# Optimization experiments

Hardware: AMD Instinct MI355X
Metric: run time of the kernel (lower is better)

## Reference

```python
import jax, jax.numpy as jnp
from jax import lax
import numpy as np

# pywt db4 filter bank (ascending order)
DEC_LO = np.array([-0.010597401784997278, 0.032883011666982945, 0.030841381835986965,
                   -0.18703481171888114, -0.02798376941698385, 0.6308807679295904,
                   0.7148465705525415, 0.23037781330885523], dtype=np.float32)
F_LEN = DEC_LO.shape[0]
_signs = ((-1.0) ** (np.arange(F_LEN) + 1)).astype(np.float32)
DEC_HI = _signs * DEC_LO[::-1]
REC_LO = DEC_LO[::-1].copy()
REC_HI = DEC_HI[::-1].copy()
# conv filters flipped -> cross-correlation kernels for lax.conv
DEC_K = np.stack([DEC_LO[::-1], DEC_HI[::-1]])[:, None, :]   # (2, 1, F): lo/hi analysis
REC_K = np.stack([REC_LO[::-1], REC_HI[::-1]])[None, :, :]   # (1, 2, F): synthesis, sums lo+hi
LEVELS = 3


def dwt_level(x, dec_k):
    """One symmetric-mode DWT level. x: (M, n) -> (cA, cD) each (M, floor((n+F-1)/2))."""
    f = dec_k.shape[-1]
    x_ext = jnp.pad(x, ((0, 0), (f - 1, f - 1)), mode='symmetric')[:, 1:]
    y = lax.conv_general_dilated(x_ext[:, None, :], dec_k, (2,), 'VALID',
                                 dimension_numbers=('NCH', 'OIH', 'NCH'))
    return y[:, 0], y[:, 1]


def idwt_level(ca, cd, rec_k, out_len):
    """One IDWT level; trims to out_len (original length at that level)."""
    f = rec_k.shape[-1]
    m, L = ca.shape
    up = jnp.zeros((m, 2, 2 * L), ca.dtype).at[:, 0, ::2].set(ca).at[:, 1, ::2].set(cd)
    y = lax.conv_general_dilated(up, rec_k, (1,), [(f - 1, f - 1)],
                                 dimension_numbers=('NCH', 'OIH', 'NCH'))[:, 0]
    s = f - 2
    return y[:, s:s + out_len]


def setup_inputs() -> dict:
    key = jax.random.key(0)
    B, N, D = 8, 4096, 768
    x = jax.random.normal(key, (B, N, D), dtype=jnp.float32)
    w_approx = jnp.ones((D,), dtype=jnp.float32)
    w_details = jnp.ones((LEVELS, D), dtype=jnp.float32)
    return {"x": x, "w_approx": w_approx, "w_details": w_details}


def reference(x, w_approx, w_details):
    B, N, D = x.shape
    dec_k = jnp.asarray(DEC_K)
    rec_k = jnp.asarray(REC_K)
    # all channels processed at once: (B, N, D) -> (B*D, N)
    sig = x.transpose(0, 2, 1).reshape(B * D, N)
    # J-level decomposition, recording per-level lengths for reconstruction
    a = sig
    lengths = []
    details = []
    for _ in range(LEVELS):
        lengths.append(a.shape[-1])
        a, d = dwt_level(a, dec_k)
        details.append(d)
    # pointwise mixing: one scalar per channel per band (matches ones(1,1,D) param sliced per-channel)
    def chan(w):  # (D,) -> (B*D, 1)
        return jnp.broadcast_to(w, (B, D)).reshape(B * D, 1)
    a = a * chan(w_approx)
    details = [d * chan(w_details[j]) for j, d in enumerate(details)]
    # reconstruction
    rec = a
    for j in reversed(range(LEVELS)):
        rec = idwt_level(rec, details[j], rec_k, lengths[j])
    rec = rec.reshape(B, D, N).transpose(0, 2, 1)
    # residual connection (dropout=0.0)
    return x + rec
```

## Files before the change

kernel.cpp:

```cpp
#include <hip/hip_runtime.h>


namespace {

constexpr int NT  = 256;
constexpr int N0  = 4096;
constexpr int DCH = 768;
constexpr int TS  = 256;
constexpr int TE  = 256;
constexpr int G   = 8;
constexpr int NDG = DCH / G;
constexpr int L1v = 2051, L2v = 1029, L3v = 518;

constexpr int NSEG = (N0 - 2 * TE) / TS;
constexpr int NINT = 8 * 3 * NSEG;

constexpr int SP = 972;
constexpr int OX = 0, OA1 = 356, OD1 = 536, OA2 = 716, OD2 = 804,
              OA3 = 892, OD3 = 932, OREC = 716;

__device__ constexpr float LO[8] = {
  -0.010597401784997278f,  0.032883011666982945f,  0.030841381835986965f,
  -0.18703481171888114f,  -0.02798376941698385f,   0.6308807679295904f,
   0.7148465705525415f,    0.23037781330885523f };
__device__ constexpr float HI[8] = {
  -0.23037781330885523f,   0.7148465705525415f,   -0.6308807679295904f,
  -0.02798376941698385f,   0.18703481171888114f,   0.030841381835986965f,
  -0.032883011666982945f, -0.010597401784997278f };
__device__ constexpr float LOF[8] = {
   0.23037781330885523f,   0.7148465705525415f,    0.6308807679295904f,
  -0.02798376941698385f,  -0.18703481171888114f,   0.030841381835986965f,
   0.032883011666982945f, -0.010597401784997278f };
__device__ constexpr float HIF[8] = {
  -0.010597401784997278f, -0.032883011666982945f,  0.030841381835986965f,
   0.18703481171888114f,  -0.02798376941698385f,  -0.6308807679295904f,
   0.7148465705525415f,   -0.23037781330885523f };

__device__ __forceinline__ int refl(int g, int n) {
  g = (g < 0) ? (-g - 1) : g;
  return (g >= n) ? (2 * n - 1 - g) : g;
}

struct Streams {
  float xa[22];
  float a1a[14], d1a[29];
  float a2a[10], d2a[13];
  float a3a[5],  d3a[5];
  float r2a[7],  r1a[11];
};

template <int SMODE>
__device__ __forceinline__ void superstep(Streams& S, float (&RR)[36],
                                          const float* __restrict__ xrow,
                                          float* __restrict__ orow, int bk8,
                                          float wa, float w0, float w1,
                                          float w2) {
#pragma unroll
  for (int i = 0; i < 16; ++i)
    S.xa[6 + i] = xrow[(long)(bk8 - 48 + i) * DCH];

#pragma unroll
  for (int u = 0; u < 2; ++u) {
#pragma unroll
    for (int j = 0; j < 4; ++j) {
      float slo = 0.f, shi = 0.f;
#pragma unroll
      for (int k = 0; k < 8; ++k) {
        const float v = S.xa[8 * u + 2 * j + k];
        slo = fmaf(LOF[k], v, slo);
        shi = fmaf(HIF[k], v, shi);
      }
      S.a1a[6 + 4 * u + j]  = slo;
      S.d1a[21 + 4 * u + j] = w0 * shi;
    }
#pragma unroll
    for (int i = 0; i < 2; ++i) {
      float slo = 0.f, shi = 0.f;
#pragma unroll
      for (int k = 0; k < 8; ++k) {
        const float v = S.a1a[4 * u + 2 * i + k];
        slo = fmaf(LOF[k], v, slo);
        shi = fmaf(HIF[k], v, shi);
      }
      S.a2a[6 + 2 * u + i] = slo;
      S.d2a[9 + 2 * u + i] = w1 * shi;
    }
    {
      float slo = 0.f, shi = 0.f;
#pragma unroll
      for (int k = 0; k < 8; ++k) {
        const float v = S.a2a[2 * u + k];
        slo = fmaf(LOF[k], v, slo);
        shi = fmaf(HIF[k], v, shi);
      }
      S.a3a[3 + u] = wa * slo;
      S.d3a[3 + u] = w2 * shi;
    }
    {
      float e = 0.f, o = 0.f;
#pragma unroll
      for (int m = 0; m < 4; ++m) {
        e = fmaf(LO[2 * m + 1], S.a3a[u + m], e);
        e = fmaf(HI[2 * m + 1], S.d3a[u + m], e);
        o = fmaf(LO[2 * m],     S.a3a[u + m], o);
        o = fmaf(HI[2 * m],     S.d3a[u + m], o);
      }
      S.r2a[3 + 2 * u]     = e;
      S.r2a[3 + 2 * u + 1] = o;
    }
#pragma unroll
    for (int h = 0; h < 2; ++h) {
      float e = 0.f, o = 0.f;
#pragma unroll
      for (int m = 0; m < 4; ++m) {
        e = fmaf(LO[2 * m + 1], S.r2a[2 * u + h + m], e);
        e = fmaf(HI[2 * m + 1], S.d2a[2 * u + h + m], e);
        o = fmaf(LO[2 * m],     S.r2a[2 * u + h + m], o);
        o = fmaf(HI[2 * m],     S.d2a[2 * u + h + m], o);
      }
      S.r1a[3 + 4 * u + 2 * h]     = e;
      S.r1a[3 + 4 * u + 2 * h + 1] = o;
    }
    if (SMODE != 0) {
#pragma unroll
      for (int tau = 0; tau < 4; ++tau) {
        bool doSt;
        if (SMODE == 2)      doSt = true;
        else if (SMODE == 1) doSt = (u == 1) && (tau >= 1);
        else                 doSt = (u == 0) || (tau == 0);
        if (doSt) {
          float e = 0.f, o = 0.f;
#pragma unroll
          for (int m = 0; m < 4; ++m) {
            e = fmaf(LO[2 * m + 1], S.r1a[4 * u + tau + m], e);
            e = fmaf(HI[2 * m + 1], S.d1a[4 * u + tau + m], e);
            o = fmaf(LO[2 * m],     S.r1a[4 * u + tau + m], o);
            o = fmaf(HI[2 * m],     S.d1a[4 * u + tau + m], o);
          }
          const long ofs = bk8 + 8 * u - 90 + 2 * tau;
          orow[ofs * DCH]       = e + RR[8 * u + 2 * tau];
          orow[(ofs + 1) * DCH] = o + RR[8 * u + 2 * tau + 1];
        }
      }
    }
  }
#pragma unroll
  for (int i = 0; i < 20; ++i) RR[i] = RR[i + 16];
#pragma unroll
  for (int i = 0; i < 16; ++i) RR[20 + i] = S.xa[i];
#pragma unroll
  for (int i = 0; i < 6; ++i)  S.xa[i]  = S.xa[i + 16];
#pragma unroll
  for (int i = 0; i < 6; ++i)  S.a1a[i] = S.a1a[i + 8];
#pragma unroll
  for (int i = 0; i < 21; ++i) S.d1a[i] = S.d1a[i + 8];
#pragma unroll
  for (int i = 0; i < 6; ++i)  S.a2a[i] = S.a2a[i + 4];
#pragma unroll
  for (int i = 0; i < 9; ++i)  S.d2a[i] = S.d2a[i + 4];
#pragma unroll
  for (int i = 0; i < 3; ++i) { S.a3a[i] = S.a3a[i + 2]; S.d3a[i] = S.d3a[i + 2]; }
#pragma unroll
  for (int i = 0; i < 3; ++i)  S.r2a[i] = S.r2a[i + 4];
#pragma unroll
  for (int i = 0; i < 3; ++i)  S.r1a[i] = S.r1a[i + 8];
}


__device__ void analyze_g(const float* __restrict__ in, int Oin,
                          float* __restrict__ oa, float* __restrict__ od,
                          int cnt, int Oout, int lenout, int i2) {
  for (int p = i2; p < cnt; p += 32) {
    const int gp = refl(Oout + p, lenout);
    const int qb = 2 * gp - 6 - Oin;
    float alo = 0.f, ahi = 0.f;
#pragma unroll
    for (int k = 0; k < 8; ++k) {
      const float v = in[qb + k];
      alo = fmaf(LOF[k], v, alo);
      ahi = fmaf(HIF[k], v, ahi);
    }
    oa[p] = alo;
    od[p] = ahi;
  }
}

__device__ void synth_g(const float* __restrict__ ca,
                        const float* __restrict__ cd, int doff,
                        float* __restrict__ o, float sa, float sd, int npair,
                        int i2) {
  for (int t = i2; t < npair; t += 32) {
    float e = 0.f, ed = 0.f, oe = 0.f, od_ = 0.f;
#pragma unroll
    for (int m = 0; m < 4; ++m) {
      e   = fmaf(LO[2 * m + 1], ca[t + m], e);
      ed  = fmaf(HI[2 * m + 1], cd[t + doff + m], ed);
      oe  = fmaf(LO[2 * m],     ca[t + m], oe);
      od_ = fmaf(HI[2 * m],     cd[t + doff + m], od_);
    }
    o[2 * t]     = sa * e  + sd * ed;
    o[2 * t + 1] = sa * oe + sd * od_;
  }
}

}

__global__ __launch_bounds__(NT) void wavemix_kernel(
    const float* __restrict__ x, const float* __restrict__ wap,
    const float* __restrict__ wdet, float* __restrict__ out) {
  __shared__ float pool[G * SP];
  const int blk = blockIdx.x;
  const int tid = threadIdx.x;

  if (blk < NINT) {
    const int wgs    = (blk & 7) * (NINT >> 3) + (blk >> 3);
    const int si     = wgs % NSEG;
    const int row    = wgs / NSEG;
    const int wgroup = row % 3;
    const int b      = row / 3;
    const int n0     = (si + 1) * TS;
    const int d      = wgroup * 256 + tid;

    const float* __restrict__ xrow = x   + ((size_t)b * N0 + n0) * DCH + d;
    float* __restrict__       orow = out + ((size_t)b * N0 + n0) * DCH + d;
    const float wa = wap[d];
    const float w0 = wdet[d];
    const float w1 = wdet[DCH + d];
    const float w2 = wdet[2 * DCH + d];

    Streams S = {};
    float RR[36];
#pragma unroll
    for (int i = 0; i < 36; ++i) RR[i] = 0.f;

    int bk8 = 0;
#pragma unroll 1
    for (int m = 0; m < 5; ++m) {
      superstep<0>(S, RR, xrow, orow, bk8, wa, w0, w1, w2);
      bk8 += 16;
    }
    superstep<1>(S, RR, xrow, orow, bk8, wa, w0, w1, w2);
    bk8 += 16;
#pragma unroll 1
    for (int m = 0; m < 15; ++m) {
      superstep<2>(S, RR, xrow, orow, bk8, wa, w0, w1, w2);
      bk8 += 16;
    }
    superstep<3>(S, RR, xrow, orow, bk8, wa, w0, w1, w2);
  } else {
    const int e    = blk - NINT;
    const int nt   = (e & 1) ? 15 : 0;
    const int rest = e >> 1;
    const int dg   = rest % NDG;
    const int b    = rest / NDG;
    const int n0   = nt * TE;
    const int d0   = dg * G;

    {
      const int q  = tid & 1;
      const int pl = tid >> 1;
      for (int p = pl; p < 352; p += 128) {
        const int g = refl(n0 - 46 + p, N0);
        const float4 v = *reinterpret_cast<const float4*>(
            x + ((size_t)b * N0 + g) * DCH + d0 + 4 * q);
        float* dst = pool + (4 * q) * SP + OX + p;
        dst[0]      = v.x;
        dst[SP]     = v.y;
        dst[2 * SP] = v.z;
        dst[3 * SP] = v.w;
      }
    }

    const int c2 = tid >> 5;
    const int i2 = tid & 31;
    float* P = pool + c2 * SP;
    const float wa = wap[d0 + c2];
    const float w2 = wdet[2 * DCH + d0 + c2];
    const float w1 = wdet[1 * DCH + d0 + c2];
    const float w0 = wdet[0 * DCH + d0 + c2];
    __syncthreads();

    analyze_g(P + OX,  n0 - 46,     P + OA1, P + OD1, 172, n0 / 2 - 20, L1v, i2);
    __syncthreads();
    analyze_g(P + OA1, n0 / 2 - 20, P + OA2, P + OD2,  82, n0 / 4 - 6,  L2v, i2);
    __syncthreads();
    analyze_g(P + OA2, n0 / 4 - 6,  P + OA3, P + OD3,  38, n0 / 8,      L3v, i2);
    __syncthreads();
    synth_g(P + OA3, P + OD3, 0, P + OA2, wa,  w2, 35, i2);
    __syncthreads();
    synth_g(P + OA2, P + OD2, 6, P + OA1, 1.f, w1, 66, i2);
    __syncthreads();
    for (int t = i2; t < 128; t += 32) {
      const float* pa = P + OA1;
      const float* pd = P + OD1;
      float e2 = 0.f, ed = 0.f, oe = 0.f, od_ = 0.f;
#pragma unroll
      for (int m = 0; m < 4; ++m) {
        e2  = fmaf(LO[2 * m + 1], pa[t + m], e2);
        ed  = fmaf(HI[2 * m + 1], pd[t + 20 + m], ed);
        oe  = fmaf(LO[2 * m],     pa[t + m], oe);
        od_ = fmaf(HI[2 * m],     pd[t + 20 + m], od_);
      }
      (P + OREC)[2 * t]     = e2 + w0 * ed  + (P + OX)[2 * t + 46];
      (P + OREC)[2 * t + 1] = oe + w0 * od_ + (P + OX)[2 * t + 47];
    }
    __syncthreads();

    {
      const int c = tid & 7;
      const int j = tid >> 3;
      const float* R = pool + c * SP + OREC;
      float* orow = out + ((size_t)b * N0 + n0) * DCH + d0 + c;
      for (int pos = j; pos < TE; pos += 32)
        orow[(size_t)pos * DCH] = R[pos];
    }
  }
}

extern "C" void kernel_launch(void* const* d_in, const int* in_sizes, int n_in,
                              void* d_out, int out_size, void* d_ws, size_t ws_size,
                              hipStream_t stream) {
  const float* x  = (const float*)d_in[0];
  const float* wa = (const float*)d_in[1];
  const float* wd = (const float*)d_in[2];
  float* out      = (float*)d_out;

  const int grid = NINT + 8 * NDG * 2;
  wavemix_kernel<<<grid, NT, 0, stream>>>(x, wa, wd, out);
}
```

Measured before the change: 53.62 us.

## Double-buffer interior input rows through LDS with float4 prefetch

Interior blocks no longer load 16 strided scalar rows straight from global memory in each superstep. A 16x256 tile is staged through a double-buffered LDS pool using float4 loads, and the next tile's loads are issued before the current step's compute so their latency is hidden. Launch bounds now request 4 blocks per SIMD-unit, which may limit registers and cause spills. Each step adds a __syncthreads, and LDS use grows to 8192 floats, which must still fit the edge-block path that reuses the pool.

After: 101.9 us. 90.0% more time.

```diff
diff --git a/kernel.cpp b/kernel.cpp
--- a/kernel.cpp
+++ b/kernel.cpp
@@ -51,13 +51,13 @@
 
 template <int SMODE>
 __device__ __forceinline__ void superstep(Streams& S, float (&RR)[36],
-                                          const float* __restrict__ xrow,
+                                          const float* __restrict__ lx,
                                           float* __restrict__ orow, int bk8,
                                           float wa, float w0, float w1,
                                           float w2) {
 #pragma unroll
   for (int i = 0; i < 16; ++i)
-    S.xa[6 + i] = xrow[(long)(bk8 - 48 + i) * DCH];
+    S.xa[6 + i] = lx[i * 256];
 
 #pragma unroll
   for (int u = 0; u < 2; ++u) {
@@ -166,6 +166,35 @@
   for (int i = 0; i < 3; ++i)  S.r1a[i] = S.r1a[i + 8];
 }
 
+template <int SMODE, bool STG>
+__device__ __forceinline__ void run_step(Streams& S, float (&RR)[36],
+                                         float* __restrict__ pool, int& cur,
+                                         int& bk8,
+                                         const float* __restrict__ gsb,
+                                         float* __restrict__ orow, int tid,
+                                         int c4, int pw, float wa, float w0,
+                                         float w1, float w2) {
+  float4 s0, s1, s2, s3;
+  if (STG) {
+    const float* g = gsb + (long)(bk8 - 32 + pw) * DCH + c4;
+    s0 = *reinterpret_cast<const float4*>(g);
+    s1 = *reinterpret_cast<const float4*>(g + (size_t)4 * DCH);
+    s2 = *reinterpret_cast<const float4*>(g + (size_t)8 * DCH);
+    s3 = *reinterpret_cast<const float4*>(g + (size_t)12 * DCH);
+  }
+  superstep<SMODE>(S, RR, pool + cur * 4096 + tid, orow, bk8, wa, w0, w1, w2);
+  if (STG) {
+    float* l = pool + (cur ^ 1) * 4096 + pw * 256 + c4;
+    *reinterpret_cast<float4*>(l)              = s0;
+    *reinterpret_cast<float4*>(l + 4 * 256)    = s1;
+    *reinterpret_cast<float4*>(l + 8 * 256)    = s2;
+    *reinterpret_cast<float4*>(l + 12 * 256)   = s3;
+    __syncthreads();
+  }
+  cur ^= 1;
+  bk8 += 16;
+}
+
 
 __device__ void analyze_g(const float* __restrict__ in, int Oin,
                           float* __restrict__ oa, float* __restrict__ od,
@@ -205,10 +234,10 @@
 
 }
 
-__global__ __launch_bounds__(NT) void wavemix_kernel(
+__global__ __launch_bounds__(NT, 4) void wavemix_kernel(
     const float* __restrict__ x, const float* __restrict__ wap,
     const float* __restrict__ wdet, float* __restrict__ out) {
-  __shared__ float pool[G * SP];
+  __shared__ float pool[8192];
   const int blk = blockIdx.x;
   const int tid = threadIdx.x;
 
@@ -219,34 +248,42 @@
     const int wgroup = row % 3;
     const int b      = row / 3;
     const int n0     = (si + 1) * TS;
-    const int d      = wgroup * 256 + tid;
-
-    const float* __restrict__ xrow = x   + ((size_t)b * N0 + n0) * DCH + d;
-    float* __restrict__       orow = out + ((size_t)b * N0 + n0) * DCH + d;
-    const float wa = wap[d];
-    const float w0 = wdet[d];
-    const float w1 = wdet[DCH + d];
-    const float w2 = wdet[2 * DCH + d];
+    const int d0     = wgroup * 256;
+
+    const float* __restrict__ gsb = x + ((size_t)b * N0 + n0) * DCH + d0;
+    float* __restrict__ orow = out + ((size_t)b * N0 + n0) * DCH + d0 + tid;
+    const float wa = wap[d0 + tid];
+    const float w0 = wdet[d0 + tid];
+    const float w1 = wdet[DCH + d0 + tid];
+    const float w2 = wdet[2 * DCH + d0 + tid];
+
+    const int c4 = 4 * (tid & 63);
+    const int pw = tid >> 6;
 
     Streams S = {};
     float RR[36];
 #pragma unroll
     for (int i = 0; i < 36; ++i) RR[i] = 0.f;
 
-    int bk8 = 0;
+    {
+      const float* g = gsb + (long)(-48 + pw) * DCH + c4;
+      float* l = pool + pw * 256 + c4;
+      *reinterpret_cast<float4*>(l)            = *reinterpret_cast<const float4*>(g);
+      *reinterpret_cast<float4*>(l + 4 * 256)  = *reinterpret_cast<const float4*>(g + (size_t)4 * DCH);
+      *reinterpret_cast<float4*>(l + 8 * 256)  = *reinterpret_cast<const float4*>(g + (size_t)8 * DCH);
+      *reinterpret_cast<float4*>(l + 12 * 256) = *reinterpret_cast<const float4*>(g + (size_t)12 * DCH);
+    }
+    __syncthreads();
+
+    int cur = 0, bk8 = 0;
 #pragma unroll 1
-    for (int m = 0; m < 5; ++m) {
-      superstep<0>(S, RR, xrow, orow, bk8, wa, w0, w1, w2);
-      bk8 += 16;
-    }
-    superstep<1>(S, RR, xrow, orow, bk8, wa, w0, w1, w2);
-    bk8 += 16;
+    for (int m = 0; m < 5; ++m)
+      run_step<0, true>(S, RR, pool, cur, bk8, gsb, orow, tid, c4, pw, wa, w0, w1, w2);
+    run_step<1, true>(S, RR, pool, cur, bk8, gsb, orow, tid, c4, pw, wa, w0, w1, w2);
 #pragma unroll 1
-    for (int m = 0; m < 15; ++m) {
-      superstep<2>(S, RR, xrow, orow, bk8, wa, w0, w1, w2);
-      bk8 += 16;
-    }
-    superstep<3>(S, RR, xrow, orow, bk8, wa, w0, w1, w2);
+    for (int m = 0; m < 15; ++m)
+      run_step<2, true>(S, RR, pool, cur, bk8, gsb, orow, tid, c4, pw, wa, w0, w1, w2);
+    run_step<3, false>(S, RR, pool, cur, bk8, gsb, orow, tid, c4, pw, wa, w0, w1, w2);
   } else {
     const int e    = blk - NINT;
     const int nt   = (e & 1) ? 15 : 0;
```
